# Optimization experiments

Hardware: AMD Instinct MI355X
Metric: run time of the kernel (lower is better)

The kernel has to match this reference:

```python
import jax, jax.numpy as jnp
import numpy as np

N_PTS = 262144
N_FREQS = 10          # positional-encoding octaves for FourierEncoder
ORDER = 16            # Chebyshev / Fourier series order
OUT_F = 3             # rgb
HIDDEN = 128
N_HIDDEN_LAYERS = 5   # 6 total layers: input layer + 5 skip layers
ENC_DIM = 3 * (1 + 2 * N_FREQS)  # 63


def _normalize(v, eps):
    # matches torch F.normalize: v / max(||v||, eps)
    return v / jnp.maximum(jnp.linalg.norm(v, axis=-1, keepdims=True), eps)


def coordinate_system(n):
    n = _normalize(n, 1e-6)
    x, y, z = n[..., 0:1], n[..., 1:2], n[..., 2:3]
    sign = jnp.where(z >= 0, 1.0, -1.0)
    s_z = sign + z
    safe = jnp.where(jnp.abs(s_z) < 1e-6, jnp.copysign(jnp.asarray(1e-6, n.dtype), s_z), s_z)
    a = -1.0 / safe
    b = x * y * a
    s = jnp.concatenate([x * x * a * sign + 1.0, b * sign, -x * sign], axis=-1)
    s = _normalize(s, 1e-6)
    t = _normalize(jnp.cross(s, n), 1e-6)
    s = _normalize(jnp.cross(n, t), 1e-6)
    return jnp.stack([s, t, n], axis=-1)  # [..., 3(world), 3(basis)]


def to_local(frame, wo):
    # (frame * wo[..., None]).sum(-2) == frame^T @ wo
    return _normalize(jnp.einsum('...ij,...i->...j', frame, wo), 1e-7)


def cos_D_phi(wo, wi):
    num = wo[..., 0:1] * wi[..., 0:1] + wo[..., 1:2] * wi[..., 1:2]
    den = jnp.sqrt((wo[..., 0:1] ** 2 + wo[..., 1:2] ** 2) *
                   (wi[..., 0:1] ** 2 + wi[..., 1:2] ** 2))
    return jnp.clip(num / den, -1.0, 1.0)


def _encode(x):
    # FourierEncoder: [x, sin(2^k x), cos(2^k x)]
    freqs = 2.0 ** jnp.arange(N_FREQS, dtype=x.dtype)  # [L]
    xb = (x[..., None, :] * freqs[:, None]).reshape(*x.shape[:-1], 3 * N_FREQS)
    return jnp.concatenate([x, jnp.sin(xb), jnp.cos(xb)], axis=-1)  # [..., 63]


def _mlp(x, W0, b0, Wh, bh, Wout, bout):
    # SkipConnMLP: 6 layers, hidden 128, encoded input re-concatenated at each hidden layer
    enc = _encode(x)
    h = jax.nn.leaky_relu(enc @ W0 + b0)
    for i in range(Wh.shape[0]):  # small fixed loop over layers
        h = jax.nn.leaky_relu(jnp.concatenate([h, enc], axis=-1) @ Wh[i] + bh[i])
    return h @ Wout + bout  # [..., OUT_F*ORDER]


def setup_inputs() -> dict:
    key = jax.random.key(0)
    ks = jax.random.split(key, 10)
    inp = {
        'x': jax.random.normal(ks[0], (N_PTS, 3), jnp.float32),
        'view': jax.random.normal(ks[1], (N_PTS, 3), jnp.float32),
        'normal': jax.random.normal(ks[2], (N_PTS, 3), jnp.float32),
        'light': jax.random.normal(ks[3], (N_PTS, 3), jnp.float32),
    }
    def xavier(k, shape):
        std = np.sqrt(2.0 / (shape[-2] + shape[-1]))
        return jax.random.normal(k, shape, jnp.float32) * std
    skip_in = HIDDEN + ENC_DIM
    inp['W0'] = xavier(ks[4], (ENC_DIM, HIDDEN))
    inp['b0'] = jnp.zeros((HIDDEN,), jnp.float32)
    inp['Wh'] = xavier(ks[5], (N_HIDDEN_LAYERS, skip_in, HIDDEN))
    inp['bh'] = jnp.zeros((N_HIDDEN_LAYERS, HIDDEN), jnp.float32)
    inp['Wout'] = xavier(ks[6], (HIDDEN, OUT_F * ORDER))
    inp['bout'] = jnp.zeros((OUT_F * ORDER,), jnp.float32)
    return inp


def reference(x, view, normal, light, W0, b0, Wh, bh, Wout, bout):
    frame = coordinate_system(normal)
    wo = to_local(frame, _normalize(view, 1e-6))
    wi = to_local(frame, light)
    cos_phi = cos_D_phi(-wi, wo)  # [N, 1]
    # unrolled Chebyshev recurrence: T_k(cos_phi) = cos(k*phi)
    cheb = [jnp.ones_like(cos_phi), cos_phi]
    for _ in range(2, ORDER):
        cheb.append(2.0 * cos_phi * cheb[-1] - cheb[-2])
    cheb = jnp.concatenate(cheb, axis=-1)  # [N, ORDER]
    coeffs = _mlp(x, W0, b0, Wh, bh, Wout, bout).reshape(*x.shape[:-1], OUT_F, ORDER)
    rgb = jnp.sum(coeffs * cheb[..., None, :], axis=-1)  # [N, 3]
    return rgb
```

## Files before the change

### kernel.cpp

```cpp
#include <hip/hip_runtime.h>
#include <hip/hip_bf16.h>

#define N_PTS    262144
#define MB       64
#define NBLOCKS  (N_PTS / MB)
#define NTHREADS 256

#define WHS_OFF    8192
#define WHS_STRIDE 24576
#define WOUTS_OFF  131072
#define WS_TOTAL   137216

typedef __bf16 bf16x8 __attribute__((ext_vector_type(8)));
typedef __bf16 bf16x4 __attribute__((ext_vector_type(4)));
typedef float  f32x4  __attribute__((ext_vector_type(4)));

__global__ __launch_bounds__(256) void prep_weights(
    const float* __restrict__ W0, const float* __restrict__ b0,
    const float* __restrict__ Wh, const float* __restrict__ bh,
    const float* __restrict__ Wout, __hip_bfloat16* __restrict__ ws)
{
    int d = blockIdx.x * 256 + threadIdx.x;
    if (d >= WS_TOTAL) return;
    int j    = d & 7;
    int lane = (d >> 3) & 63;
    int kin  = ((lane >> 4) & 3) * 8 + j;
    int nlo  = lane & 15;
    float val;
    if (d < WHS_OFF) {
        int f = d >> 9;
        int k = (f >> 3) * 32 + kin;
        int n = (f & 7) * 16 + nlo;
        val = (k < 63) ? W0[k * 128 + n] : b0[n];
    } else if (d < WOUTS_OFF) {
        int local = d - WHS_OFF;
        int layer = local / WHS_STRIDE;
        int f = (local % WHS_STRIDE) >> 9;
        int k = (f >> 3) * 32 + kin;
        int n = (f & 7) * 16 + nlo;
        val = (k < 191) ? Wh[(layer * 191 + k) * 128 + n] : bh[layer * 128 + n];
    } else {
        int f = (d - WOUTS_OFF) >> 9;
        int k = (f / 3) * 32 + kin;
        int n = (f % 3) * 16 + nlo;
        val = Wout[k * 48 + n];
    }
    ws[d] = __float2bfloat16(val);
}


__device__ __forceinline__ unsigned pack2bf(float a, float b)
{
    __hip_bfloat162 h = __float22bfloat162_rn(float2{a, b});
    return *reinterpret_cast<unsigned*>(&h);
}

template<int KS>
__device__ __forceinline__ void mm_gw(
    const __hip_bfloat16* __restrict__ actb, int ptbase, int acol0, int ksbase,
    const __hip_bfloat16* __restrict__ wsrc, int ug,
    int m, int g, int lane, f32x4 (&acc)[4][2])
{
#pragma unroll
    for (int ks = 0; ks < KS; ++ks) {
        int col = acol0 + (ksbase + ks) * 32 + g * 8;
        int poff = (((col >> 3) ^ (m & 7)) << 3);
        bf16x8 a[4];
#pragma unroll
        for (int mt = 0; mt < 4; ++mt)
            a[mt] = *reinterpret_cast<const bf16x8*>(
                wsrc + (((ksbase + ks) * 8 + ug * 4 + mt) * 64 + lane) * 8);
        bf16x8 b[2];
#pragma unroll
        for (int nf = 0; nf < 2; ++nf)
            b[nf] = *reinterpret_cast<const bf16x8*>(
                actb + (ptbase + nf * 16 + m) * 192 + poff);
        __builtin_amdgcn_s_setprio(1);
#pragma unroll
        for (int mt = 0; mt < 4; ++mt)
#pragma unroll
            for (int nf = 0; nf < 2; ++nf)
                acc[mt][nf] = __builtin_amdgcn_mfma_f32_16x16x32_bf16(a[mt], b[nf], acc[mt][nf], 0, 0, 0);
        __builtin_amdgcn_s_setprio(0);
    }
}

__device__ __forceinline__ void zero_acc(f32x4 (&acc)[4][2])
{
#pragma unroll
    for (int i = 0; i < 4; ++i)
#pragma unroll
        for (int k = 0; k < 2; ++k)
            acc[i][k] = f32x4{0.f, 0.f, 0.f, 0.f};
}

__device__ __forceinline__ void writeback_gw(__hip_bfloat16* actb, f32x4 (&acc)[4][2],
                                             int ptbase, int ug, int m, int g)
{
#pragma unroll
    for (int mt = 0; mt < 4; ++mt) {
        int chunk = (ug * 4 + mt) * 2 + (g >> 1);
#pragma unroll
        for (int nf = 0; nf < 2; ++nf) {
            int pt = ptbase + nf * 16 + m;
            float v0 = acc[mt][nf][0]; v0 = fmaxf(v0, 0.01f * v0);
            float v1 = acc[mt][nf][1]; v1 = fmaxf(v1, 0.01f * v1);
            float v2 = acc[mt][nf][2]; v2 = fmaxf(v2, 0.01f * v2);
            float v3 = acc[mt][nf][3]; v3 = fmaxf(v3, 0.01f * v3);
            uint2 pk; pk.x = pack2bf(v0, v1); pk.y = pack2bf(v2, v3);
            *reinterpret_cast<uint2*>(
                actb + pt * 192 + ((chunk ^ (pt & 7)) << 3) + (g & 1) * 4) = pk;
        }
    }
}

__global__ __launch_bounds__(NTHREADS, 4) void fused_kernel(
    const float* __restrict__ x, const float* __restrict__ view,
    const float* __restrict__ normal, const float* __restrict__ light,
    const float* __restrict__ bout, const __hip_bfloat16* __restrict__ ws,
    float* __restrict__ out)
{
    __shared__ __align__(16) __hip_bfloat16 s_act[MB * 192];
    __shared__ __align__(16) __hip_bfloat16 chebt[MB * 16];

    const int tid  = threadIdx.x;
    const int lane = tid & 63;
    const int wave = tid >> 6;
    const int m = lane & 15;
    const int g = lane >> 4;
    const int ug = wave & 1;
    const int pg = wave >> 1;
    const int ptbase = pg * 32;
    const int block0 = blockIdx.x * MB;

    if (tid >= 192) {
        int pt  = tid - 192;
        int pid = block0 + pt;
        float nx = normal[pid*3+0], ny = normal[pid*3+1], nz = normal[pid*3+2];
        float vx = view[pid*3+0],   vy = view[pid*3+1],   vz = view[pid*3+2];
        float lx = light[pid*3+0],  ly = light[pid*3+1],  lz = light[pid*3+2];

        float inv = 1.f / fmaxf(sqrtf(nx*nx + ny*ny + nz*nz), 1e-6f);
        nx *= inv; ny *= inv; nz *= inv;
        float sgn = (nz >= 0.f) ? 1.f : -1.f;
        float s_z = sgn + nz;
        float safe = (fabsf(s_z) < 1e-6f) ? copysignf(1e-6f, s_z) : s_z;
        float a = -1.f / safe;
        float b = nx * ny * a;
        float sx = nx*nx*a*sgn + 1.f, sy = b*sgn, sz = -nx*sgn;
        inv = 1.f / fmaxf(sqrtf(sx*sx + sy*sy + sz*sz), 1e-6f); sx*=inv; sy*=inv; sz*=inv;
        float tx = sy*nz - sz*ny, ty = sz*nx - sx*nz, tz = sx*ny - sy*nx;
        inv = 1.f / fmaxf(sqrtf(tx*tx + ty*ty + tz*tz), 1e-6f); tx*=inv; ty*=inv; tz*=inv;
        sx = ny*tz - nz*ty; sy = nz*tx - nx*tz; sz = nx*ty - ny*tx;
        inv = 1.f / fmaxf(sqrtf(sx*sx + sy*sy + sz*sz), 1e-6f); sx*=inv; sy*=inv; sz*=inv;

        inv = 1.f / fmaxf(sqrtf(vx*vx + vy*vy + vz*vz), 1e-6f); vx*=inv; vy*=inv; vz*=inv;
        float wox = sx*vx + sy*vy + sz*vz;
        float woy = tx*vx + ty*vy + tz*vz;
        float woz = nx*vx + ny*vy + nz*vz;
        inv = 1.f / fmaxf(sqrtf(wox*wox + woy*woy + woz*woz), 1e-7f); wox*=inv; woy*=inv;
        float wix = sx*lx + sy*ly + sz*lz;
        float wiy = tx*lx + ty*ly + tz*lz;
        float wiz = nx*lx + ny*ly + nz*lz;
        inv = 1.f / fmaxf(sqrtf(wix*wix + wiy*wiy + wiz*wiz), 1e-7f); wix*=inv; wiy*=inv;
        float axn = -wix, ayn = -wiy;
        float num = axn*wox + ayn*woy;
        float den = sqrtf((axn*axn + ayn*ayn) * (wox*wox + woy*woy));
        float cp = fminf(fmaxf(num / den, -1.f), 1.f);

        chebt[pt*16 + 0] = __float2bfloat16(1.f);
        chebt[pt*16 + 1] = __float2bfloat16(cp);
        float t0 = 1.f, t1 = cp;
        for (int k = 2; k < 16; ++k) {
            float t2 = 2.f*cp*t1 - t0;
            chebt[pt*16 + k] = __float2bfloat16(t2);
            t0 = t1; t1 = t2;
        }
    }

    if (tid < 2 * MB) {
        int pt  = tid >> 1;
        int sub = tid & 1;
        int pid = block0 + pt;
        float px = x[pid*3+0], py = x[pid*3+1], pz = x[pid*3+2];
        const int sw = pt & 7;
        __hip_bfloat16* ar = &s_act[pt * 192];
#define ENC_ST(cidx, val) ar[(((((cidx)+128) >> 3) ^ sw) << 3) + (((cidx)+128) & 7)] = __float2bfloat16(val)
        if (sub == 0) {
            ENC_ST(0, px); ENC_ST(1, py); ENC_ST(2, pz);
        } else {
            ENC_ST(63, 1.0f);
        }
#pragma unroll
        for (int ff = 0; ff < 5; ++ff) {
            int f = sub * 5 + ff;
            float fr = (float)(1 << f);
            float s0, c0, s1, c1, s2, c2;
            __sincosf(px * fr, &s0, &c0);
            __sincosf(py * fr, &s1, &c1);
            __sincosf(pz * fr, &s2, &c2);
            ENC_ST(3  + f*3 + 0, s0);
            ENC_ST(3  + f*3 + 1, s1);
            ENC_ST(3  + f*3 + 2, s2);
            ENC_ST(33 + f*3 + 0, c0);
            ENC_ST(33 + f*3 + 1, c1);
            ENC_ST(33 + f*3 + 2, c2);
        }
#undef ENC_ST
    }
    __syncthreads();

    float4 T_reg;
    {
        bf16x4 tv = *reinterpret_cast<const bf16x4*>(&chebt[(wave * 16 + m) * 16 + g * 4]);
        T_reg.x = (float)tv[0];
        T_reg.y = (float)tv[1];
        T_reg.z = (float)tv[2];
        T_reg.w = (float)tv[3];
    }

    f32x4 acc[4][2];

    zero_acc(acc);
    mm_gw<2>(s_act, ptbase, 128, 0, ws, ug, m, g, lane, acc);
    writeback_gw(s_act, acc, ptbase, ug, m, g);
    __syncthreads();

    for (int L = 0; L < 5; ++L) {
        const __hip_bfloat16* wsrc = ws + WHS_OFF + L * WHS_STRIDE;
        zero_acc(acc);
        mm_gw<2>(s_act, ptbase, 0, 4, wsrc, ug, m, g, lane, acc);
        mm_gw<4>(s_act, ptbase, 0, 0, wsrc, ug, m, g, lane, acc);
        __syncthreads();
        writeback_gw(s_act, acc, ptbase, ug, m, g);
        __syncthreads();
    }

    {
        f32x4 oacc[3];
#pragma unroll
        for (int c = 0; c < 3; ++c) oacc[c] = f32x4{0.f, 0.f, 0.f, 0.f};
        const int ptb = wave * 16;
        const __hip_bfloat16* wo = ws + WOUTS_OFF;
#pragma unroll
        for (int ks = 0; ks < 4; ++ks) {
            int col = ks * 32 + g * 8;
            int poff = (((col >> 3) ^ (m & 7)) << 3);
            bf16x8 b = *reinterpret_cast<const bf16x8*>(s_act + (ptb + m) * 192 + poff);
#pragma unroll
            for (int c = 0; c < 3; ++c) {
                bf16x8 a = *reinterpret_cast<const bf16x8*>(wo + ((ks * 3 + c) * 64 + lane) * 8);
                oacc[c] = __builtin_amdgcn_mfma_f32_16x16x32_bf16(a, b, oacc[c], 0, 0, 0);
            }
        }

#pragma unroll
        for (int c = 0; c < 3; ++c) {
            float partial = 0.f;
#pragma unroll
            for (int r = 0; r < 4; ++r)
                partial += (oacc[c][r] + bout[c * 16 + g * 4 + r]) * (&T_reg.x)[r];
            partial += __shfl_xor(partial, 16, 64);
            partial += __shfl_xor(partial, 32, 64);
            if (g == 0)
                out[(block0 + ptb + m) * 3 + c] = partial;
        }
    }
}

extern "C" void kernel_launch(void* const* d_in, const int* in_sizes, int n_in,
                              void* d_out, int out_size, void* d_ws, size_t ws_size,
                              hipStream_t stream)
{
    const float* x      = (const float*)d_in[0];
    const float* view   = (const float*)d_in[1];
    const float* normal = (const float*)d_in[2];
    const float* light  = (const float*)d_in[3];
    const float* W0     = (const float*)d_in[4];
    const float* b0     = (const float*)d_in[5];
    const float* Wh     = (const float*)d_in[6];
    const float* bh     = (const float*)d_in[7];
    const float* Wout   = (const float*)d_in[8];
    const float* bout   = (const float*)d_in[9];
    float* out = (float*)d_out;
    __hip_bfloat16* ws = (__hip_bfloat16*)d_ws;

    hipLaunchKernelGGL(prep_weights, dim3(WS_TOTAL / 256 + 1), dim3(256), 0, stream,
                       W0, b0, Wh, bh, Wout, ws);
    hipLaunchKernelGGL(fused_kernel, dim3(NBLOCKS), dim3(NTHREADS), 0, stream,
                       x, view, normal, light, bout, ws, out);
}
```

Before: 165.5 us.

## Double points per block to reuse weight fragments across more MFMA tiles

Raises the block tile from 64 to 128 points, so each wave computes a 64x64 output tile (4x4 MFMA accumulators) instead of 64x32. Each weight fragment loaded from global memory now feeds twice as many MFMAs, which halves weight traffic per point. The shading prologue moves to threads 0-127, and the Chebyshev values are read per point in the epilogue rather than held in registers through the MLP. In exchange it doubles accumulator registers and shared memory per block, lowers the launch-bounds occupancy hint from 4 to 3, and halves the number of blocks.

Result: faster. 152.0 us (-8.1%).

```diff
diff --git a/kernel.cpp b/kernel.cpp
--- a/kernel.cpp
+++ b/kernel.cpp
@@ -2,7 +2,7 @@
 #include <hip/hip_bf16.h>
 
 #define N_PTS    262144
-#define MB       64
+#define MB       128
 #define NBLOCKS  (N_PTS / MB)
 #define NTHREADS 256
 
@@ -59,7 +59,7 @@
 __device__ __forceinline__ void mm_gw(
     const __hip_bfloat16* __restrict__ actb, int ptbase, int acol0, int ksbase,
     const __hip_bfloat16* __restrict__ wsrc, int ug,
-    int m, int g, int lane, f32x4 (&acc)[4][2])
+    int m, int g, int lane, f32x4 (&acc)[4][4])
 {
 #pragma unroll
     for (int ks = 0; ks < KS; ++ks) {
@@ -70,38 +70,38 @@
         for (int mt = 0; mt < 4; ++mt)
             a[mt] = *reinterpret_cast<const bf16x8*>(
                 wsrc + (((ksbase + ks) * 8 + ug * 4 + mt) * 64 + lane) * 8);
-        bf16x8 b[2];
-#pragma unroll
-        for (int nf = 0; nf < 2; ++nf)
+        bf16x8 b[4];
+#pragma unroll
+        for (int nf = 0; nf < 4; ++nf)
             b[nf] = *reinterpret_cast<const bf16x8*>(
                 actb + (ptbase + nf * 16 + m) * 192 + poff);
         __builtin_amdgcn_s_setprio(1);
 #pragma unroll
         for (int mt = 0; mt < 4; ++mt)
 #pragma unroll
-            for (int nf = 0; nf < 2; ++nf)
+            for (int nf = 0; nf < 4; ++nf)
                 acc[mt][nf] = __builtin_amdgcn_mfma_f32_16x16x32_bf16(a[mt], b[nf], acc[mt][nf], 0, 0, 0);
         __builtin_amdgcn_s_setprio(0);
     }
 }
 
-__device__ __forceinline__ void zero_acc(f32x4 (&acc)[4][2])
+__device__ __forceinline__ void zero_acc(f32x4 (&acc)[4][4])
 {
 #pragma unroll
     for (int i = 0; i < 4; ++i)
 #pragma unroll
-        for (int k = 0; k < 2; ++k)
+        for (int k = 0; k < 4; ++k)
             acc[i][k] = f32x4{0.f, 0.f, 0.f, 0.f};
 }
 
-__device__ __forceinline__ void writeback_gw(__hip_bfloat16* actb, f32x4 (&acc)[4][2],
+__device__ __forceinline__ void writeback_gw(__hip_bfloat16* actb, f32x4 (&acc)[4][4],
                                              int ptbase, int ug, int m, int g)
 {
 #pragma unroll
     for (int mt = 0; mt < 4; ++mt) {
         int chunk = (ug * 4 + mt) * 2 + (g >> 1);
 #pragma unroll
-        for (int nf = 0; nf < 2; ++nf) {
+        for (int nf = 0; nf < 4; ++nf) {
             int pt = ptbase + nf * 16 + m;
             float v0 = acc[mt][nf][0]; v0 = fmaxf(v0, 0.01f * v0);
             float v1 = acc[mt][nf][1]; v1 = fmaxf(v1, 0.01f * v1);
@@ -114,7 +114,7 @@
     }
 }
 
-__global__ __launch_bounds__(NTHREADS, 4) void fused_kernel(
+__global__ __launch_bounds__(NTHREADS, 3) void fused_kernel(
     const float* __restrict__ x, const float* __restrict__ view,
     const float* __restrict__ normal, const float* __restrict__ light,
     const float* __restrict__ bout, const __hip_bfloat16* __restrict__ ws,
@@ -130,12 +130,11 @@
     const int g = lane >> 4;
     const int ug = wave & 1;
     const int pg = wave >> 1;
-    const int ptbase = pg * 32;
+    const int ptbase = pg * 64;
     const int block0 = blockIdx.x * MB;
 
-    if (tid >= 192) {
-        int pt  = tid - 192;
-        int pid = block0 + pt;
+    if (tid < MB) {
+        int pid = block0 + tid;
         float nx = normal[pid*3+0], ny = normal[pid*3+1], nz = normal[pid*3+2];
         float vx = view[pid*3+0],   vy = view[pid*3+1],   vz = view[pid*3+2];
         float lx = light[pid*3+0],  ly = light[pid*3+1],  lz = light[pid*3+2];
@@ -168,12 +167,12 @@
         float den = sqrtf((axn*axn + ayn*ayn) * (wox*wox + woy*woy));
         float cp = fminf(fmaxf(num / den, -1.f), 1.f);
 
-        chebt[pt*16 + 0] = __float2bfloat16(1.f);
-        chebt[pt*16 + 1] = __float2bfloat16(cp);
+        chebt[tid*16 + 0] = __float2bfloat16(1.f);
+        chebt[tid*16 + 1] = __float2bfloat16(cp);
         float t0 = 1.f, t1 = cp;
         for (int k = 2; k < 16; ++k) {
             float t2 = 2.f*cp*t1 - t0;
-            chebt[pt*16 + k] = __float2bfloat16(t2);
+            chebt[tid*16 + k] = __float2bfloat16(t2);
             t0 = t1; t1 = t2;
         }
     }
@@ -210,16 +209,7 @@
     }
     __syncthreads();
 
-    float4 T_reg;
-    {
-        bf16x4 tv = *reinterpret_cast<const bf16x4*>(&chebt[(wave * 16 + m) * 16 + g * 4]);
-        T_reg.x = (float)tv[0];
-        T_reg.y = (float)tv[1];
-        T_reg.z = (float)tv[2];
-        T_reg.w = (float)tv[3];
-    }
-
-    f32x4 acc[4][2];
+    f32x4 acc[4][4];
 
     zero_acc(acc);
     mm_gw<2>(s_act, ptbase, 128, 0, ws, ug, m, g, lane, acc);
@@ -237,33 +227,53 @@
     }
 
     {
-        f32x4 oacc[3];
-#pragma unroll
-        for (int c = 0; c < 3; ++c) oacc[c] = f32x4{0.f, 0.f, 0.f, 0.f};
-        const int ptb = wave * 16;
+        f32x4 oacc[3][2];
+#pragma unroll
+        for (int c = 0; c < 3; ++c)
+#pragma unroll
+            for (int nt = 0; nt < 2; ++nt)
+                oacc[c][nt] = f32x4{0.f, 0.f, 0.f, 0.f};
+        const int ptb = wave * 32;
         const __hip_bfloat16* wo = ws + WOUTS_OFF;
 #pragma unroll
         for (int ks = 0; ks < 4; ++ks) {
             int col = ks * 32 + g * 8;
             int poff = (((col >> 3) ^ (m & 7)) << 3);
-            bf16x8 b = *reinterpret_cast<const bf16x8*>(s_act + (ptb + m) * 192 + poff);
+            bf16x8 b[2];
+#pragma unroll
+            for (int nt = 0; nt < 2; ++nt)
+                b[nt] = *reinterpret_cast<const bf16x8*>(s_act + (ptb + nt * 16 + m) * 192 + poff);
 #pragma unroll
             for (int c = 0; c < 3; ++c) {
                 bf16x8 a = *reinterpret_cast<const bf16x8*>(wo + ((ks * 3 + c) * 64 + lane) * 8);
-                oacc[c] = __builtin_amdgcn_mfma_f32_16x16x32_bf16(a, b, oacc[c], 0, 0, 0);
+#pragma unroll
+                for (int nt = 0; nt < 2; ++nt)
+                    oacc[c][nt] = __builtin_amdgcn_mfma_f32_16x16x32_bf16(a, b[nt], oacc[c][nt], 0, 0, 0);
             }
         }
 
 #pragma unroll
-        for (int c = 0; c < 3; ++c) {
-            float partial = 0.f;
-#pragma unroll
-            for (int r = 0; r < 4; ++r)
-                partial += (oacc[c][r] + bout[c * 16 + g * 4 + r]) * (&T_reg.x)[r];
-            partial += __shfl_xor(partial, 16, 64);
-            partial += __shfl_xor(partial, 32, 64);
-            if (g == 0)
-                out[(block0 + ptb + m) * 3 + c] = partial;
+        for (int nt = 0; nt < 2; ++nt) {
+            int pt = ptb + nt * 16 + m;
+            float4 T_reg;
+            {
+                bf16x4 tv = *reinterpret_cast<const bf16x4*>(&chebt[pt * 16 + g * 4]);
+                T_reg.x = (float)tv[0];
+                T_reg.y = (float)tv[1];
+                T_reg.z = (float)tv[2];
+                T_reg.w = (float)tv[3];
+            }
+#pragma unroll
+            for (int c = 0; c < 3; ++c) {
+                float partial = 0.f;
+#pragma unroll
+                for (int r = 0; r < 4; ++r)
+                    partial += (oacc[c][nt][r] + bout[c * 16 + g * 4 + r]) * (&T_reg.x)[r];
+                partial += __shfl_xor(partial, 16, 64);
+                partial += __shfl_xor(partial, 32, 64);
+                if (g == 0)
+                    out[(block0 + pt) * 3 + c] = partial;
+            }
         }
     }
 }
```
